# Optimization experiments

Hardware: AMD Instinct MI355X
Metric: run time of the kernel (lower is better)

Reference implementation:

```python
import jax, jax.numpy as jnp
import numpy as np

BATCH, SEQ, D_IN, D_STATE = 8, 4096, 1024, 64


def setup_inputs() -> dict:
    key = jax.random.key(0)
    ks = jax.random.split(key, 3)
    u = jax.random.normal(ks[0], (BATCH, SEQ, D_IN), dtype=jnp.float32)
    log_A = jnp.zeros((D_STATE,), dtype=jnp.float32)
    B = jax.random.normal(ks[1], (D_STATE, D_IN), dtype=jnp.float32) * 0.01
    C = jax.random.normal(ks[2], (D_IN, D_STATE), dtype=jnp.float32) * 0.01
    D = jnp.ones((D_IN,), dtype=jnp.float32)
    log_delta = jnp.zeros((D_IN,), dtype=jnp.float32)
    return {"u": u, "log_A": log_A, "B": B, "C": C, "D": D, "log_delta": log_delta}


def reference(u, log_A, B, C, D, log_delta):
    batch, seq_len, input_dim = u.shape
    state_dim = log_A.shape[0]
    delta = jax.nn.softplus(log_delta)                      # [I]
    A = -jnp.exp(log_A)                                     # [N]
    A_bar = jnp.exp(delta[:, None] * A[None, :])            # [I, N]
    A_bar_state = A_bar.mean(axis=0)                        # [N]
    B_bar = B * delta[None, :]                              # [N, I]
    # Precompute input projections for all timesteps: [B, T, N]
    Bu = jnp.einsum('ni,bti->btn', B_bar, u)
    x0 = jnp.zeros((batch, state_dim), dtype=u.dtype)

    def step(x, bu_t):
        x = x * A_bar_state[None, :] + bu_t
        return x, x

    _, xs = jax.lax.scan(step, x0, jnp.swapaxes(Bu, 0, 1))  # xs: [T, B, N]
    xs = jnp.swapaxes(xs, 0, 1)                             # [B, T, N]
    y = jnp.einsum('in,btn->bti', C, xs) + D[None, None, :] * u
    return y
```

## Files before the change

kernel.cpp:

```cpp
#include <hip/hip_runtime.h>
#include <hip/hip_bf16.h>
#include <cstdint>

#define BATCH 8
#define SEQ   4096
#define DIN   1024
#define DST   64
#define CHUNK 64
#define NC    (SEQ/CHUNK)

typedef __attribute__((ext_vector_type(8))) short short8;
typedef __attribute__((ext_vector_type(4))) short short4v;
typedef __attribute__((ext_vector_type(4))) float f32x4;

__device__ __forceinline__ short f2bf(float f) {
    union { float f; unsigned u; } v; v.f = f;
    unsigned r = v.u + 0x7fffu + ((v.u >> 16) & 1u);
    return (short)(r >> 16);
}
__device__ __forceinline__ float softplus_f(float x) {
    return (x > 20.f) ? x : log1pf(expf(x));
}

__global__ void ssm_k0(const float* __restrict__ logA, const float* __restrict__ Bm,
                       const float* __restrict__ Cm, const float* __restrict__ logdelta,
                       short* __restrict__ Bb, short* __restrict__ Cb,
                       float* __restrict__ a_o, float* __restrict__ l2a_o,
                       float* __restrict__ aL_o)
{
    __shared__ float red[256];
    int blk = blockIdx.x, tid = threadIdx.x;
    if (blk < DST) {
        int n = blk;
        float An = -expf(logA[n]);
        float acc = 0.f;
        #pragma unroll
        for (int ii = 0; ii < DIN/256; ++ii) {
            int i = ii*256 + tid;
            float dlt = softplus_f(logdelta[i]);
            Bb[n*DIN + i] = f2bf(Bm[n*DIN + i] * dlt);
            acc += expf(dlt * An);
        }
        red[tid] = acc; __syncthreads();
        for (int s = 128; s > 0; s >>= 1) {
            if (tid < s) red[tid] += red[tid + s];
            __syncthreads();
        }
        if (tid == 0) {
            float a = red[0] * (1.f/DIN);
            a_o[n]   = a;
            l2a_o[n] = log2f(a);
            float p = a;
            #pragma unroll
            for (int q = 0; q < 6; ++q) p = p*p;
            aL_o[n] = p;
        }
    } else {
        int base = (blk - DST) * (DIN*DST/16);
        for (int e = tid; e < DIN*DST/16; e += 256)
            Cb[base + e] = f2bf(Cm[base + e]);
    }
}

__global__ __launch_bounds__(256) void ssm_k1(
    const float* __restrict__ u, const short* __restrict__ Bb,
    const float* __restrict__ a_i, float* __restrict__ xloc, float* __restrict__ carry)
{
    int blk = blockIdx.x;
    int b = blk >> 6, c = blk & (NC-1);
    int tid = threadIdx.x;
    int w = tid >> 6, lane = tid & 63;
    int m = lane & 15, quad = lane >> 4;

    long row = ((long)b << 12) + (c << 6) + (w << 4) + m;
    const float* up = u + row * DIN + quad * 8;

    f32x4 acc0 = {0,0,0,0}, acc1 = {0,0,0,0}, acc2 = {0,0,0,0}, acc3 = {0,0,0,0};

    #pragma unroll 4
    for (int ks = 0; ks < DIN/32; ++ks) {
        const float4* uv = (const float4*)(up + ks*32);
        float4 ua = uv[0];
        float4 ub = uv[1];
        short8 af;
        af[0]=f2bf(ua.x); af[1]=f2bf(ua.y); af[2]=f2bf(ua.z); af[3]=f2bf(ua.w);
        af[4]=f2bf(ub.x); af[5]=f2bf(ub.y); af[6]=f2bf(ub.z); af[7]=f2bf(ub.w);
        const short* bbase = Bb + ks*32 + quad*8;
        short8 b0 = *(const short8*)(bbase + ( 0 + m)*DIN);
        short8 b1 = *(const short8*)(bbase + (16 + m)*DIN);
        short8 b2 = *(const short8*)(bbase + (32 + m)*DIN);
        short8 b3 = *(const short8*)(bbase + (48 + m)*DIN);
        acc0 = __builtin_amdgcn_mfma_f32_16x16x32_bf16(af, b0, acc0, 0,0,0);
        acc1 = __builtin_amdgcn_mfma_f32_16x16x32_bf16(af, b1, acc1, 0,0,0);
        acc2 = __builtin_amdgcn_mfma_f32_16x16x32_bf16(af, b2, acc2, 0,0,0);
        acc3 = __builtin_amdgcn_mfma_f32_16x16x32_bf16(af, b3, acc3, 0,0,0);
    }

    __shared__ float bu[CHUNK][DST];
    int trow = (w << 4) + (quad << 2);
    #pragma unroll
    for (int r = 0; r < 4; ++r) {
        bu[trow + r][ 0 + m] = acc0[r];
        bu[trow + r][16 + m] = acc1[r];
        bu[trow + r][32 + m] = acc2[r];
        bu[trow + r][48 + m] = acc3[r];
    }
    __syncthreads();

    if (tid < DST) {
        int n = tid;
        float an = a_i[n];
        float x = 0.f;
        float* xp = xloc + (((long)b << 12) + (c << 6)) * DST + n;
        #pragma unroll 8
        for (int t = 0; t < CHUNK; ++t) {
            x = x * an + bu[t][n];
            xp[(long)t * DST] = x;
        }
        carry[(b * NC + c) * DST + n] = x;
    }
}

__global__ void ssm_k2(const float* __restrict__ carry, const float* __restrict__ aL,
                       float* __restrict__ Xin)
{
    int b = blockIdx.x, n = threadIdx.x;
    float x = 0.f, al = aL[n];
    for (int c = 0; c < NC; ++c) {
        Xin[(b*NC + c)*DST + n] = x;
        x = x * al + carry[(b*NC + c)*DST + n];
    }
}

__global__ __launch_bounds__(256) void ssm_k3(
    const float* __restrict__ u, const float* __restrict__ xloc,
    const float* __restrict__ Xin, const float* __restrict__ l2a,
    const short* __restrict__ Cb, const float* __restrict__ D,
    float* __restrict__ y)
{
    int tblk = blockIdx.x;
    long t0 = (long)tblk << 4;
    int b = (int)(t0 >> 12);
    int tloc0 = (int)(t0 & (SEQ-1));
    int chunk = tloc0 >> 6;
    int jbase = tloc0 & (CHUNK-1);

    __shared__ short xb[16][DST];

    int tid = threadIdx.x;
    {
        int m  = tid >> 4;
        int n0 = (tid & 15) * 4;
        long t = t0 + m;
        int j  = jbase + m;
        float4 xv = *(const float4*)(xloc + t*DST + n0);
        float4 xi = *(const float4*)(Xin + (long)(b*NC + chunk)*DST + n0);
        float4 la = *(const float4*)(l2a + n0);
        float jp = (float)(j + 1);
        short4v xs;
        xs[0] = f2bf(xv.x + exp2f(jp*la.x)*xi.x);
        xs[1] = f2bf(xv.y + exp2f(jp*la.y)*xi.y);
        xs[2] = f2bf(xv.z + exp2f(jp*la.z)*xi.z);
        xs[3] = f2bf(xv.w + exp2f(jp*la.w)*xi.w);
        *(short4v*)(&xb[m][n0]) = xs;
    }
    __syncthreads();

    int w = tid >> 6, lane = tid & 63;
    int n16 = lane & 15, quad = lane >> 4;

    short8 a0 = *(const short8*)(&xb[n16][ 0 + quad*8]);
    short8 a1 = *(const short8*)(&xb[n16][32 + quad*8]);

    #pragma unroll 4
    for (int ii = 0; ii < 16; ++ii) {
        int i0 = (ii*4 + w) * 16;
        int i  = i0 + n16;
        const short* cb = Cb + (long)i*DST + quad*8;
        short8 b0 = *(const short8*)(cb);
        short8 b1 = *(const short8*)(cb + 32);
        f32x4 acc = {0,0,0,0};
        acc = __builtin_amdgcn_mfma_f32_16x16x32_bf16(a0, b0, acc, 0,0,0);
        acc = __builtin_amdgcn_mfma_f32_16x16x32_bf16(a1, b1, acc, 0,0,0);
        float Di = D[i];
        #pragma unroll
        for (int r = 0; r < 4; ++r) {
            long t = t0 + quad*4 + r;
            long off = t*DIN + i;
            y[off] = acc[r] + Di * u[off];
        }
    }
}

extern "C" void kernel_launch(void* const* d_in, const int* in_sizes, int n_in,
                              void* d_out, int out_size, void* d_ws, size_t ws_size,
                              hipStream_t stream)
{
    const float* u        = (const float*)d_in[0];
    const float* logA     = (const float*)d_in[1];
    const float* Bm       = (const float*)d_in[2];
    const float* Cm       = (const float*)d_in[3];
    const float* D        = (const float*)d_in[4];
    const float* logdelta = (const float*)d_in[5];
    float* y = (float*)d_out;

    char* ws = (char*)d_ws;
    float* xloc  = (float*)(ws);
    float* carry = (float*)(ws + 8u*1024*1024);
    float* Xin   = (float*)(ws + 8u*1024*1024 + 128*1024);
    short* Bb    = (short*)(ws + 8u*1024*1024 + 256*1024);
    short* Cb    = (short*)(ws + 8u*1024*1024 + 384*1024);
    float* a_o   = (float*)(ws + 8u*1024*1024 + 512*1024);
    float* l2a_o = a_o + 64;
    float* aL_o  = a_o + 128;

    hipLaunchKernelGGL(ssm_k0, dim3(DST + 16), dim3(256), 0, stream,
                       logA, Bm, Cm, logdelta, Bb, Cb, a_o, l2a_o, aL_o);
    hipLaunchKernelGGL(ssm_k1, dim3(BATCH*NC), dim3(256), 0, stream,
                       u, Bb, a_o, xloc, carry);
    hipLaunchKernelGGL(ssm_k2, dim3(BATCH), dim3(DST), 0, stream,
                       carry, aL_o, Xin);
    hipLaunchKernelGGL(ssm_k3, dim3((BATCH*SEQ)/16), dim3(256), 0, stream,
                       u, xloc, Xin, l2a_o, Cb, D, y);
}
```

Before: 307.5 us.

## Split K across waves in projection, vectorize output stores, preload carries

The Bu projection kernel now runs 512 threads, with two wave groups each covering half of the input dimension. Their partial results go into two shared-memory buffers that are summed inside the sequential scan. The output kernel swaps the MFMA operand order so each lane owns four consecutive output columns, which turns scalar u/D loads and y stores into float4 accesses. The carry-scan kernel loads all chunk carries into registers before its serial loop. Together these aim to raise parallelism and memory coalescing, at the cost of more registers and shared memory in the projection kernel.

Result: slower. 320.0 us (+4.1%).

```diff
diff --git a/kernel.cpp b/kernel.cpp
--- a/kernel.cpp
+++ b/kernel.cpp
@@ -62,7 +62,7 @@
     }
 }
 
-__global__ __launch_bounds__(256) void ssm_k1(
+__global__ __launch_bounds__(512) void ssm_k1(
     const float* __restrict__ u, const short* __restrict__ Bb,
     const float* __restrict__ a_i, float* __restrict__ xloc, float* __restrict__ carry)
 {
@@ -70,22 +70,24 @@
     int b = blk >> 6, c = blk & (NC-1);
     int tid = threadIdx.x;
     int w = tid >> 6, lane = tid & 63;
+    int wr = w & 3, wk = w >> 2;
     int m = lane & 15, quad = lane >> 4;
 
-    long row = ((long)b << 12) + (c << 6) + (w << 4) + m;
-    const float* up = u + row * DIN + quad * 8;
+    long row = ((long)b << 12) + (c << 6) + (wr << 4) + m;
+    const float* up  = u  + row * DIN + wk*(DIN/2) + quad * 8;
+    const short* bb0 = Bb + wk*(DIN/2) + quad * 8;
 
     f32x4 acc0 = {0,0,0,0}, acc1 = {0,0,0,0}, acc2 = {0,0,0,0}, acc3 = {0,0,0,0};
 
     #pragma unroll 4
-    for (int ks = 0; ks < DIN/32; ++ks) {
+    for (int ks = 0; ks < DIN/64; ++ks) {
         const float4* uv = (const float4*)(up + ks*32);
         float4 ua = uv[0];
         float4 ub = uv[1];
         short8 af;
         af[0]=f2bf(ua.x); af[1]=f2bf(ua.y); af[2]=f2bf(ua.z); af[3]=f2bf(ua.w);
         af[4]=f2bf(ub.x); af[5]=f2bf(ub.y); af[6]=f2bf(ub.z); af[7]=f2bf(ub.w);
-        const short* bbase = Bb + ks*32 + quad*8;
+        const short* bbase = bb0 + ks*32;
         short8 b0 = *(const short8*)(bbase + ( 0 + m)*DIN);
         short8 b1 = *(const short8*)(bbase + (16 + m)*DIN);
         short8 b2 = *(const short8*)(bbase + (32 + m)*DIN);
@@ -96,14 +98,14 @@
         acc3 = __builtin_amdgcn_mfma_f32_16x16x32_bf16(af, b3, acc3, 0,0,0);
     }
 
-    __shared__ float bu[CHUNK][DST];
-    int trow = (w << 4) + (quad << 2);
+    __shared__ float bu[2][CHUNK][DST];
+    int trow = (wr << 4) + (quad << 2);
     #pragma unroll
     for (int r = 0; r < 4; ++r) {
-        bu[trow + r][ 0 + m] = acc0[r];
-        bu[trow + r][16 + m] = acc1[r];
-        bu[trow + r][32 + m] = acc2[r];
-        bu[trow + r][48 + m] = acc3[r];
+        bu[wk][trow + r][ 0 + m] = acc0[r];
+        bu[wk][trow + r][16 + m] = acc1[r];
+        bu[wk][trow + r][32 + m] = acc2[r];
+        bu[wk][trow + r][48 + m] = acc3[r];
     }
     __syncthreads();
 
@@ -114,7 +116,7 @@
         float* xp = xloc + (((long)b << 12) + (c << 6)) * DST + n;
         #pragma unroll 8
         for (int t = 0; t < CHUNK; ++t) {
-            x = x * an + bu[t][n];
+            x = x * an + (bu[0][t][n] + bu[1][t][n]);
             xp[(long)t * DST] = x;
         }
         carry[(b * NC + c) * DST + n] = x;
@@ -125,17 +127,22 @@
                        float* __restrict__ Xin)
 {
     int b = blockIdx.x, n = threadIdx.x;
+    float cr[NC];
+    #pragma unroll
+    for (int c = 0; c < NC; ++c)
+        cr[c] = carry[(b*NC + c)*DST + n];
     float x = 0.f, al = aL[n];
+    #pragma unroll
     for (int c = 0; c < NC; ++c) {
         Xin[(b*NC + c)*DST + n] = x;
-        x = x * al + carry[(b*NC + c)*DST + n];
+        x = x * al + cr[c];
     }
 }
 
 __global__ __launch_bounds__(256) void ssm_k3(
     const float* __restrict__ u, const float* __restrict__ xloc,
     const float* __restrict__ Xin, const float* __restrict__ l2a,
-    const short* __restrict__ Cb, const float* __restrict__ D,
+    const short* __restrict__ Cb, const float* __restrict__ Dv,
     float* __restrict__ y)
 {
     int tblk = blockIdx.x;
@@ -167,28 +174,33 @@
     __syncthreads();
 
     int w = tid >> 6, lane = tid & 63;
-    int n16 = lane & 15, quad = lane >> 4;
-
-    short8 a0 = *(const short8*)(&xb[n16][ 0 + quad*8]);
-    short8 a1 = *(const short8*)(&xb[n16][32 + quad*8]);
+    int l16 = lane & 15, quad = lane >> 4;
+
+    short8 x0 = *(const short8*)(&xb[l16][ 0 + quad*8]);
+    short8 x1 = *(const short8*)(&xb[l16][32 + quad*8]);
+
+    long trow = t0 + l16;
+    const float* urow = u + trow*DIN;
+    float* yrow = y + trow*DIN;
 
     #pragma unroll 4
     for (int ii = 0; ii < 16; ++ii) {
         int i0 = (ii*4 + w) * 16;
-        int i  = i0 + n16;
-        const short* cb = Cb + (long)i*DST + quad*8;
-        short8 b0 = *(const short8*)(cb);
-        short8 b1 = *(const short8*)(cb + 32);
+        const short* cb = Cb + (long)(i0 + l16)*DST + quad*8;
+        short8 c0 = *(const short8*)(cb);
+        short8 c1 = *(const short8*)(cb + 32);
         f32x4 acc = {0,0,0,0};
-        acc = __builtin_amdgcn_mfma_f32_16x16x32_bf16(a0, b0, acc, 0,0,0);
-        acc = __builtin_amdgcn_mfma_f32_16x16x32_bf16(a1, b1, acc, 0,0,0);
-        float Di = D[i];
-        #pragma unroll
-        for (int r = 0; r < 4; ++r) {
-            long t = t0 + quad*4 + r;
-            long off = t*DIN + i;
-            y[off] = acc[r] + Di * u[off];
-        }
+        acc = __builtin_amdgcn_mfma_f32_16x16x32_bf16(c0, x0, acc, 0,0,0);
+        acc = __builtin_amdgcn_mfma_f32_16x16x32_bf16(c1, x1, acc, 0,0,0);
+        int ib = i0 + (quad << 2);
+        float4 dd = *(const float4*)(Dv + ib);
+        float4 uu = *(const float4*)(urow + ib);
+        float4 o;
+        o.x = acc[0] + dd.x*uu.x;
+        o.y = acc[1] + dd.y*uu.y;
+        o.z = acc[2] + dd.z*uu.z;
+        o.w = acc[3] + dd.w*uu.w;
+        *(float4*)(yrow + ib) = o;
     }
 }
 
@@ -216,7 +228,7 @@
 
     hipLaunchKernelGGL(ssm_k0, dim3(DST + 16), dim3(256), 0, stream,
                        logA, Bm, Cm, logdelta, Bb, Cb, a_o, l2a_o, aL_o);
-    hipLaunchKernelGGL(ssm_k1, dim3(BATCH*NC), dim3(256), 0, stream,
+    hipLaunchKernelGGL(ssm_k1, dim3(BATCH*NC), dim3(512), 0, stream,
                        u, Bb, a_o, xloc, carry);
     hipLaunchKernelGGL(ssm_k2, dim3(BATCH), dim3(DST), 0, stream,
                        carry, aL_o, Xin);
```
